# Performance work log

Measured on AMD Instinct MI355X. Metric: run time of the kernel, lower is better.

The kernel has to match this reference:

```python
import jax, jax.numpy as jnp
import numpy as np

N = 25000      # nodes
E = 400000     # edges
IN = 1024      # in_channels
FC = 128       # feature_channels
ADD = 20       # additional_channels
MID = (FC + ADD) // 4   # 37, fc1 output (heads=4)
OUT = 3
EPS = 1e-5
NEG_SLOPE = 0.01


def setup_inputs() -> dict:
    key = jax.random.key(0)
    ks = jax.random.split(key, 16)
    d = {}
    d["features"] = jax.random.normal(ks[0], (N, IN), dtype=jnp.float32)
    d["edges"] = jax.random.randint(ks[1], (2, E), 0, N, dtype=jnp.int64)
    d["edges2"] = jax.random.randint(ks[2], (2, 1000), 0, N, dtype=jnp.int64)
    d["edge_features"] = jax.random.normal(ks[3], (E, 1), dtype=jnp.float32)
    d["additional_feature"] = jax.random.normal(ks[4], (N, ADD), dtype=jnp.float32)
    # SAGEConv params: lin_l (neighbor path, with bias), lin_r (root path, no bias)
    s = 1.0 / np.sqrt(IN)
    d["Wl"] = jax.random.uniform(ks[5], (FC, IN), jnp.float32, -s, s)
    d["bl"] = jax.random.uniform(ks[6], (FC,), jnp.float32, -s, s)
    d["Wr"] = jax.random.uniform(ks[7], (FC, IN), jnp.float32, -s, s)
    s1 = 1.0 / np.sqrt(FC + ADD)
    d["W1"] = jax.random.uniform(ks[8], (MID, FC + ADD), jnp.float32, -s1, s1)
    d["b1"] = jax.random.uniform(ks[9], (MID,), jnp.float32, -s1, s1)
    s2 = 1.0 / np.sqrt(MID)
    d["W2"] = jax.random.uniform(ks[10], (OUT, MID), jnp.float32, -s2, s2)
    d["b2"] = jax.random.uniform(ks[11], (OUT,), jnp.float32, -s2, s2)
    # BatchNorm1d (eval mode -> running stats)
    d["gamma"] = jnp.ones((MID,), jnp.float32)
    d["beta"] = jnp.zeros((MID,), jnp.float32)
    d["run_mean"] = jax.random.normal(ks[12], (MID,), dtype=jnp.float32) * 0.1
    d["run_var"] = jnp.abs(jax.random.normal(ks[13], (MID,), dtype=jnp.float32)) * 0.1 + 1.0
    return d


def reference(features, edges, edges2, edge_features, additional_feature,
              Wl, bl, Wr, W1, b1, W2, b2, gamma, beta, run_mean, run_var):
    src, dst = edges[0], edges[1]  # PyG: messages flow source -> target
    # scatter-mean of neighbor features onto targets
    agg = jax.ops.segment_sum(features[src], dst, num_segments=N)        # [N, IN]
    deg = jax.ops.segment_sum(jnp.ones((E,), features.dtype), dst, num_segments=N)
    agg = agg / jnp.maximum(deg, 1.0)[:, None]
    # SAGEConv: lin_l(mean_neigh) + lin_r(x)
    x = agg @ Wl.T + bl + features @ Wr.T                                 # [N, FC]
    x = jnp.where(x >= 0, x, NEG_SLOPE * x)                               # leaky_relu
    # dropout is identity in eval mode
    x = jnp.concatenate([x, additional_feature], axis=1) @ W1.T + b1      # [N, MID]
    x = jnp.maximum(x, 0.0)                                               # relu
    x = gamma * (x - run_mean) * jax.lax.rsqrt(run_var + EPS) + beta      # BN eval
    return x @ W2.T + b2                                                  # [N, OUT]
```

## Files before the change

kernel.cpp:

```cpp
#include <hip/hip_runtime.h>

#define N_NODES 25000
#define N_EDGES 400000
#define IN_CH 1024
#define FC 128
#define ADD_CH 20
#define XCH 148
#define MID 37
#define OUT_CH 3
#define MAXDEG 64
#define CSTRIDE 16

typedef short bf16x8 __attribute__((ext_vector_type(8)));
typedef float f32x4 __attribute__((ext_vector_type(4)));

__device__ __forceinline__ float bflo(unsigned int v) {
    return __builtin_bit_cast(float, v << 16);
}
__device__ __forceinline__ float bfhi(unsigned int v) {
    return __builtin_bit_cast(float, v & 0xffff0000u);
}
__device__ __forceinline__ unsigned int cvtpk(float a, float b) {
    unsigned int r;
    asm("v_cvt_pk_bf16_f32 %0, %1, %2" : "=v"(r) : "v"(a), "v"(b));
    return r;
}

__device__ __forceinline__ void gload16(const void* g, void* l) {
    __builtin_amdgcn_global_load_lds(
        (const __attribute__((address_space(1))) unsigned int*)g,
        (__attribute__((address_space(3))) unsigned int*)l,
        16, 0, 0);
}

#define WSWZ_B 16
#define ZERO_B 49

__global__ __launch_bounds__(512) void prep(const float* __restrict__ Wl,
                                            const float* __restrict__ Wr,
                                            ushort* __restrict__ Wpk,
                                            int* __restrict__ cursor) {
    int b = blockIdx.x, t = threadIdx.x;
    if (b < WSWZ_B) {
        int w = t >> 6, lane = t & 63, l15 = lane & 15, q8 = (lane >> 4) * 8;
        int ch = b * 16 + l15;
        const float* src = (ch < FC) ? (Wl + (size_t)ch * IN_CH)
                                     : (Wr + (size_t)(ch - FC) * IN_CH);
        #pragma unroll
        for (int j = 0; j < 4; ++j) {
            int kt = w * 4 + j;
            float4 lo = *(const float4*)(src + kt * 32 + q8);
            float4 hi = *(const float4*)(src + kt * 32 + q8 + 4);
            uint4 pk;
            pk.x = cvtpk(lo.x, lo.y); pk.y = cvtpk(lo.z, lo.w);
            pk.z = cvtpk(hi.x, hi.y); pk.w = cvtpk(hi.z, hi.w);
            ((uint4*)Wpk)[((size_t)kt * 16 + b) * 64 + lane] = pk;
        }
    } else {
        int i = (b - WSWZ_B) * 512 + t;
        if (i < N_NODES) {
            uint4 z = {0, 0, 0, 0};
            uint4* dst = (uint4*)(cursor + (size_t)i * CSTRIDE);
            dst[0] = z; dst[1] = z; dst[2] = z; dst[3] = z;
        }
    }
}

#define GEMM_B 391
#define BUILD_B 196

__global__ __launch_bounds__(512, 4) void gemm_build(const float* __restrict__ A,
                                                     const ushort* __restrict__ Wpk,
                                                     ushort* __restrict__ Py,
                                                     ushort* __restrict__ Pz,
                                                     const int* __restrict__ edges,
                                                     int* __restrict__ cursor,
                                                     int* __restrict__ col) {
    __shared__ uint4 LDS[3][1536];
    int b = blockIdx.x, t = threadIdx.x;
    if (b >= GEMM_B) {
        int base = (b - GEMM_B) * 2048 + t;
        int src[4], dst[4], pos[4];
        #pragma unroll
        for (int k = 0; k < 4; ++k) {
            int e = base + k * 512;
            bool v = (e < N_EDGES);
            dst[k] = v ? edges[N_EDGES + e] : 0;
            src[k] = v ? edges[e] : 0;
        }
        #pragma unroll
        for (int k = 0; k < 4; ++k) {
            int e = base + k * 512;
            if (e < N_EDGES)
                pos[k] = atomicAdd(&cursor[(size_t)dst[k] * CSTRIDE], 1);
        }
        #pragma unroll
        for (int k = 0; k < 4; ++k) {
            int e = base + k * 512;
            if (e < N_EDGES && pos[k] < MAXDEG)
                col[dst[k] * MAXDEG + pos[k]] = src[k];
        }
        return;
    }
    int m0 = b * 64;

    int ga = t >> 7, hq = (t >> 6) & 1, la = t & 63;
    int nodeA = m0 + ga * 16 + (la & 15);
    if (nodeA >= N_NODES) nodeA = N_NODES - 1;
    const float* Asrc = A + (size_t)nodeA * IN_CH + (la >> 4) * 8 + hq * 4;
    const uint4* Wg = (const uint4*)Wpk;
    int tb = t & ~63;

    int w = t >> 6, lane = t & 63;
    int wm = w >> 2, wn = w & 3;
    int l15 = lane & 15, q = lane >> 4;

    f32x4 acc[4][2] = {};

    gload16(Wg + t,        &LDS[0][tb]);
    gload16(Wg + 512 + t,  &LDS[0][512 + tb]);
    gload16(Asrc,          &LDS[0][1024 + tb]);
    gload16(Wg + 1024 + t,       &LDS[1][tb]);
    gload16(Wg + 1024 + 512 + t, &LDS[1][512 + tb]);
    gload16(Asrc + 32,           &LDS[1][1024 + tb]);

    #define COMPUTE(bc)                                                           \
    {                                                                             \
        bf16x8 wf[4];                                                             \
        _Pragma("unroll")                                                         \
        for (int i = 0; i < 4; ++i)                                               \
            wf[i] = *(const bf16x8*)&LDS[bc][(wn * 4 + i) * 64 + lane];           \
        bf16x8 af[2];                                                             \
        _Pragma("unroll")                                                         \
        for (int g2 = 0; g2 < 2; ++g2) {                                          \
            f32x4 lo = *(const f32x4*)&LDS[bc][1024 + ((wm * 2 + g2) * 2 + 0) * 64 + lane]; \
            f32x4 hi = *(const f32x4*)&LDS[bc][1024 + ((wm * 2 + g2) * 2 + 1) * 64 + lane]; \
            uint4 pk;                                                             \
            pk.x = cvtpk(lo[0], lo[1]); pk.y = cvtpk(lo[2], lo[3]);               \
            pk.z = cvtpk(hi[0], hi[1]); pk.w = cvtpk(hi[2], hi[3]);               \
            af[g2] = __builtin_bit_cast(bf16x8, pk);                              \
        }                                                                         \
        _Pragma("unroll")                                                         \
        for (int i = 0; i < 4; ++i)                                               \
            _Pragma("unroll")                                                     \
            for (int g2 = 0; g2 < 2; ++g2)                                        \
                acc[i][g2] = __builtin_amdgcn_mfma_f32_16x16x32_bf16(wf[i], af[g2], acc[i][g2], 0, 0, 0); \
    }

    int bc = 0, bs = 2;
    for (int c = 0; c < 30; ++c) {
        const uint4* ws = Wg + (size_t)(c + 2) * 1024;
        gload16(ws + t,       &LDS[bs][tb]);
        gload16(ws + 512 + t, &LDS[bs][512 + tb]);
        gload16(Asrc + (size_t)(c + 2) * 32, &LDS[bs][1024 + tb]);
        asm volatile("s_waitcnt vmcnt(6)" ::: "memory");
        __builtin_amdgcn_sched_barrier(0);
        __builtin_amdgcn_s_barrier();
        __builtin_amdgcn_sched_barrier(0);
        COMPUTE(bc);
        __builtin_amdgcn_s_barrier();
        __builtin_amdgcn_sched_barrier(0);
        bc = (bc == 2) ? 0 : bc + 1;
        bs = (bs == 2) ? 0 : bs + 1;
    }
    asm volatile("s_waitcnt vmcnt(3)" ::: "memory");
    __builtin_amdgcn_sched_barrier(0);
    __builtin_amdgcn_s_barrier();
    __builtin_amdgcn_sched_barrier(0);
    COMPUTE(bc);
    bc = (bc == 2) ? 0 : bc + 1;
    asm volatile("s_waitcnt vmcnt(0)" ::: "memory");
    __builtin_amdgcn_sched_barrier(0);
    __builtin_amdgcn_s_barrier();
    __builtin_amdgcn_sched_barrier(0);
    COMPUTE(bc);
    #undef COMPUTE

    #pragma unroll
    for (int g2 = 0; g2 < 2; ++g2) {
        int node = m0 + wm * 32 + g2 * 16 + l15;
        if (node < N_NODES) {
            ushort* base = (wn < 2) ? (Py + (size_t)node * FC + (wn & 1) * 64 + q * 4)
                                    : (Pz + (size_t)node * FC + (wn & 1) * 64 + q * 4);
            #pragma unroll
            for (int i = 0; i < 4; ++i) {
                f32x4 v = acc[i][g2];
                uint2 pk;
                pk.x = cvtpk(v[0], v[1]);
                pk.y = cvtpk(v[2], v[3]);
                *(uint2*)(base + i * 16) = pk;
            }
        }
    }
}

__global__ __launch_bounds__(512) void fused_tail(const ushort* __restrict__ Py,
                                                  const ushort* __restrict__ Pz,
                                                  const int* __restrict__ deg,
                                                  const int* __restrict__ col,
                                                  const float* __restrict__ addf,
                                                  const float* __restrict__ bl,
                                                  const float* __restrict__ W1,
                                                  const float* __restrict__ b1,
                                                  const float* __restrict__ W2,
                                                  const float* __restrict__ b2,
                                                  const float* __restrict__ gamma,
                                                  const float* __restrict__ beta,
                                                  const float* __restrict__ rmean,
                                                  const float* __restrict__ rvar,
                                                  float* __restrict__ out) {
    __shared__ float W1s[XCH][MID + 3];
    __shared__ float xbuf[8][XCH + 4];
    __shared__ float hbuf[8][MID + 3];
    int t = threadIdx.x;
    for (int idx = t; idx < MID * XCH; idx += 512) {
        int j = idx / XCH, k = idx - j * XCH;
        W1s[k][j] = W1[idx];
    }
    __syncthreads();
    int w = t >> 6, lane = t & 63;
    int n = blockIdx.x * 8 + w;
    bool valid = (n < N_NODES);
    int d = valid ? deg[(size_t)n * CSTRIDE] : 0;
    if (d > MAXDEG) d = MAXDEG;
    int g = lane >> 4, c16 = lane & 15;
    float s[8] = {0.f, 0.f, 0.f, 0.f, 0.f, 0.f, 0.f, 0.f};
    if (d > 0) {
        int cidx = col[n * MAXDEG + (lane < d ? lane : 0)];
        for (int i = 0; i < d; i += 16) {
            int e[4];
            uint4 v[4];
            #pragma unroll
            for (int j = 0; j < 4; ++j) {
                int ee = i + g + j * 4;
                e[j] = __shfl(cidx, (ee < d) ? ee : 0);
            }
            #pragma unroll
            for (int j = 0; j < 4; ++j)
                v[j] = *(const uint4*)&Py[(size_t)e[j] * FC + c16 * 8];
            #pragma unroll
            for (int j = 0; j < 4; ++j) {
                if (i + g + j * 4 < d) {
                    s[0] += bflo(v[j].x); s[1] += bfhi(v[j].x);
                    s[2] += bflo(v[j].y); s[3] += bfhi(v[j].y);
                    s[4] += bflo(v[j].z); s[5] += bfhi(v[j].z);
                    s[6] += bflo(v[j].w); s[7] += bfhi(v[j].w);
                }
            }
        }
        #pragma unroll
        for (int r = 0; r < 8; ++r) {
            s[r] += __shfl_xor(s[r], 16);
            s[r] += __shfl_xor(s[r], 32);
        }
    }
    if (valid) {
        if (lane < 16) {
            #pragma unroll
            for (int r = 0; r < 8; ++r) xbuf[w][lane * 8 + r] = s[r];
        }
        float invd = 1.0f / (float)(d > 1 ? d : 1);
        unsigned int vr = *(const unsigned int*)&Pz[(size_t)n * FC + lane * 2];
        float x0 = xbuf[w][2 * lane] * invd + bl[2 * lane] + bflo(vr);
        float x1 = xbuf[w][2 * lane + 1] * invd + bl[2 * lane + 1] + bfhi(vr);
        x0 = (x0 >= 0.f) ? x0 : 0.01f * x0;
        x1 = (x1 >= 0.f) ? x1 : 0.01f * x1;
        xbuf[w][2 * lane] = x0;
        xbuf[w][2 * lane + 1] = x1;
        if (lane < ADD_CH) xbuf[w][FC + lane] = addf[(size_t)n * ADD_CH + lane];
        if (lane < MID) {
            float h = b1[lane];
            #pragma unroll 4
            for (int k = 0; k < XCH; ++k) h += W1s[k][lane] * xbuf[w][k];
            h = fmaxf(h, 0.0f);
            h = gamma[lane] * (h - rmean[lane]) * rsqrtf(rvar[lane] + 1e-5f) + beta[lane];
            hbuf[w][lane] = h;
        }
        if (lane < OUT_CH) {
            float o = b2[lane];
            #pragma unroll
            for (int j = 0; j < MID; ++j) o += W2[lane * MID + j] * hbuf[w][j];
            out[(size_t)n * OUT_CH + lane] = o;
        }
    }
}


extern "C" void kernel_launch(void* const* d_in, const int* in_sizes, int n_in,
                              void* d_out, int out_size, void* d_ws, size_t ws_size,
                              hipStream_t stream) {
    const float* features = (const float*)d_in[0];
    const int*   edges    = (const int*)d_in[1];
    const float* addf     = (const float*)d_in[4];
    const float* Wl       = (const float*)d_in[5];
    const float* bl       = (const float*)d_in[6];
    const float* Wr       = (const float*)d_in[7];
    const float* W1       = (const float*)d_in[8];
    const float* b1       = (const float*)d_in[9];
    const float* W2       = (const float*)d_in[10];
    const float* b2       = (const float*)d_in[11];
    const float* gamma    = (const float*)d_in[12];
    const float* beta     = (const float*)d_in[13];
    const float* rmean    = (const float*)d_in[14];
    const float* rvar     = (const float*)d_in[15];
    float* out = (float*)d_out;

    char* ws = (char*)d_ws;
    size_t off = 0;
    ushort* Py = (ushort*)(ws + off);     off += (size_t)N_NODES * FC * 2;
    ushort* Pz = (ushort*)(ws + off);     off += (size_t)N_NODES * FC * 2;
    ushort* Wpk = (ushort*)(ws + off);    off += (size_t)32 * 16 * 64 * 16;
    int* cursor = (int*)(ws + off);       off += (size_t)N_NODES * CSTRIDE * 4;
    int* col = (int*)(ws + off);          off += (size_t)N_NODES * MAXDEG * 4;

    prep<<<WSWZ_B + ZERO_B, 512, 0, stream>>>(Wl, Wr, Wpk, cursor);

    gemm_build<<<GEMM_B + BUILD_B, 512, 0, stream>>>(features, Wpk, Py, Pz,
                                                     edges, cursor, col);

    fused_tail<<<(N_NODES + 7) / 8, 512, 0, stream>>>(Py, Pz, cursor, col, addf, bl,
                                                      W1, b1, W2, b2, gamma, beta,
                                                      rmean, rvar, out);
}
```

Measured before the change: 255.0 us.

## Load weight fragments directly into registers and repartition warps over output columns

Weight tiles are no longer staged through LDS. Each wave now loads its own weight fragments straight into VGPRs with global_load_dwordx4, triple-buffered in registers, and only the fp32 A tile stays in LDS. The wave-to-output mapping changes so each wave covers all 64 rows and 32 output columns, which removes the LDS reads and writes for weights and shrinks LDS to a third. In exchange it uses more registers per thread for the in-flight weight buffers, and every wave re-reads the shared A tile from LDS four times, which may affect occupancy and LDS bandwidth.

```diff
diff --git a/kernel.cpp b/kernel.cpp
--- a/kernel.cpp
+++ b/kernel.cpp
@@ -13,6 +13,7 @@
 
 typedef short bf16x8 __attribute__((ext_vector_type(8)));
 typedef float f32x4 __attribute__((ext_vector_type(4)));
+typedef unsigned int u32x4 __attribute__((ext_vector_type(4)));
 
 __device__ __forceinline__ float bflo(unsigned int v) {
     return __builtin_bit_cast(float, v << 16);
@@ -76,7 +77,7 @@
                                                      const int* __restrict__ edges,
                                                      int* __restrict__ cursor,
                                                      int* __restrict__ col) {
-    __shared__ uint4 LDS[3][1536];
+    __shared__ uint4 LDS[3][512];
     int b = blockIdx.x, t = threadIdx.x;
     if (b >= GEMM_B) {
         int base = (b - GEMM_B) * 2048 + t;
@@ -103,92 +104,93 @@
         return;
     }
     int m0 = b * 64;
-
-    int ga = t >> 7, hq = (t >> 6) & 1, la = t & 63;
-    int nodeA = m0 + ga * 16 + (la & 15);
+    int w = t >> 6, lane = t & 63;
+    int l15 = lane & 15, q = lane >> 4;
+    int tb = t & ~63;
+
+    int ga = t >> 7, hq = (t >> 6) & 1;
+    int nodeA = m0 + ga * 16 + l15;
     if (nodeA >= N_NODES) nodeA = N_NODES - 1;
-    const float* Asrc = A + (size_t)nodeA * IN_CH + (la >> 4) * 8 + hq * 4;
-    const uint4* Wg = (const uint4*)Wpk;
-    int tb = t & ~63;
-
-    int w = t >> 6, lane = t & 63;
-    int wm = w >> 2, wn = w & 3;
-    int l15 = lane & 15, q = lane >> 4;
-
-    f32x4 acc[4][2] = {};
-
-    gload16(Wg + t,        &LDS[0][tb]);
-    gload16(Wg + 512 + t,  &LDS[0][512 + tb]);
-    gload16(Asrc,          &LDS[0][1024 + tb]);
-    gload16(Wg + 1024 + t,       &LDS[1][tb]);
-    gload16(Wg + 1024 + 512 + t, &LDS[1][512 + tb]);
-    gload16(Asrc + 32,           &LDS[1][1024 + tb]);
-
-    #define COMPUTE(bc)                                                           \
+    const float* Asrc = A + (size_t)nodeA * IN_CH + q * 8 + hq * 4;
+
+    unsigned voff0 = (unsigned)(w * 128 + lane) * 16u;
+
+    f32x4 acc[2][4] = {};
+    u32x4 wA0, wA1, wB0, wB1, wC0, wC1;
+
+    #define ISSUE_W(R0, R1, vo)                                                   \
+        asm volatile("global_load_dwordx4 %0, %2, %3\n\t"                         \
+                     "global_load_dwordx4 %1, %2, %3 offset:1024"                 \
+                     : "=&v"(R0), "=&v"(R1) : "v"(vo), "s"(Wpk) : "memory");
+
+    gload16(Asrc, &LDS[0][tb]);
+    ISSUE_W(wA0, wA1, voff0)
+    gload16(Asrc + 32, &LDS[1][tb]);
+    { unsigned vo = voff0 + 16384u; ISSUE_W(wB0, wB1, vo) }
+
+    #define COMPUTE(W0r, W1r, cb)                                                 \
     {                                                                             \
-        bf16x8 wf[4];                                                             \
+        bf16x8 wf0 = __builtin_bit_cast(bf16x8, W0r);                             \
+        bf16x8 wf1 = __builtin_bit_cast(bf16x8, W1r);                             \
         _Pragma("unroll")                                                         \
-        for (int i = 0; i < 4; ++i)                                               \
-            wf[i] = *(const bf16x8*)&LDS[bc][(wn * 4 + i) * 64 + lane];           \
-        bf16x8 af[2];                                                             \
-        _Pragma("unroll")                                                         \
-        for (int g2 = 0; g2 < 2; ++g2) {                                          \
-            f32x4 lo = *(const f32x4*)&LDS[bc][1024 + ((wm * 2 + g2) * 2 + 0) * 64 + lane]; \
-            f32x4 hi = *(const f32x4*)&LDS[bc][1024 + ((wm * 2 + g2) * 2 + 1) * 64 + lane]; \
-            uint4 pk;                                                             \
-            pk.x = cvtpk(lo[0], lo[1]); pk.y = cvtpk(lo[2], lo[3]);               \
-            pk.z = cvtpk(hi[0], hi[1]); pk.w = cvtpk(hi[2], hi[3]);               \
-            af[g2] = __builtin_bit_cast(bf16x8, pk);                              \
+        for (int g = 0; g < 4; ++g) {                                             \
+            f32x4 lo = *(const f32x4*)&LDS[cb][g * 128 + lane];                   \
+            f32x4 hi = *(const f32x4*)&LDS[cb][g * 128 + 64 + lane];              \
+            uint4 pk_;                                                            \
+            pk_.x = cvtpk(lo[0], lo[1]); pk_.y = cvtpk(lo[2], lo[3]);             \
+            pk_.z = cvtpk(hi[0], hi[1]); pk_.w = cvtpk(hi[2], hi[3]);             \
+            bf16x8 af = __builtin_bit_cast(bf16x8, pk_);                          \
+            acc[0][g] = __builtin_amdgcn_mfma_f32_16x16x32_bf16(wf0, af, acc[0][g], 0, 0, 0); \
+            acc[1][g] = __builtin_amdgcn_mfma_f32_16x16x32_bf16(wf1, af, acc[1][g], 0, 0, 0); \
         }                                                                         \
-        _Pragma("unroll")                                                         \
-        for (int i = 0; i < 4; ++i)                                               \
-            _Pragma("unroll")                                                     \
-            for (int g2 = 0; g2 < 2; ++g2)                                        \
-                acc[i][g2] = __builtin_amdgcn_mfma_f32_16x16x32_bf16(wf[i], af[g2], acc[i][g2], 0, 0, 0); \
-    }
-
-    int bc = 0, bs = 2;
-    for (int c = 0; c < 30; ++c) {
-        const uint4* ws = Wg + (size_t)(c + 2) * 1024;
-        gload16(ws + t,       &LDS[bs][tb]);
-        gload16(ws + 512 + t, &LDS[bs][512 + tb]);
-        gload16(Asrc + (size_t)(c + 2) * 32, &LDS[bs][1024 + tb]);
-        asm volatile("s_waitcnt vmcnt(6)" ::: "memory");
-        __builtin_amdgcn_sched_barrier(0);
-        __builtin_amdgcn_s_barrier();
-        __builtin_amdgcn_sched_barrier(0);
-        COMPUTE(bc);
-        __builtin_amdgcn_s_barrier();
-        __builtin_amdgcn_sched_barrier(0);
-        bc = (bc == 2) ? 0 : bc + 1;
-        bs = (bs == 2) ? 0 : bs + 1;
+    }
+
+    #define STEP(c, WS0, WS1, WC0, WC1, SBUF, CBUF)                               \
+    {                                                                             \
+        gload16(Asrc + (size_t)((c) + 2) * 32, &LDS[SBUF][tb]);                   \
+        unsigned vo = voff0 + (unsigned)((c) + 2) * 16384u;                       \
+        ISSUE_W(WS0, WS1, vo)                                                     \
+        asm volatile("s_waitcnt vmcnt(6)" ::: "memory");                          \
+        __builtin_amdgcn_sched_barrier(0);                                        \
+        __builtin_amdgcn_s_barrier();                                             \
+        __builtin_amdgcn_sched_barrier(0);                                        \
+        COMPUTE(WC0, WC1, CBUF);                                                  \
+        __builtin_amdgcn_s_barrier();                                             \
+        __builtin_amdgcn_sched_barrier(0);                                        \
+    }
+
+    for (int cc = 0; cc < 30; cc += 3) {
+        STEP(cc,     wC0, wC1, wA0, wA1, 2, 0)
+        STEP(cc + 1, wA0, wA1, wB0, wB1, 0, 1)
+        STEP(cc + 2, wB0, wB1, wC0, wC1, 1, 2)
     }
     asm volatile("s_waitcnt vmcnt(3)" ::: "memory");
     __builtin_amdgcn_sched_barrier(0);
     __builtin_amdgcn_s_barrier();
     __builtin_amdgcn_sched_barrier(0);
-    COMPUTE(bc);
-    bc = (bc == 2) ? 0 : bc + 1;
+    COMPUTE(wA0, wA1, 0);
     asm volatile("s_waitcnt vmcnt(0)" ::: "memory");
     __builtin_amdgcn_sched_barrier(0);
     __builtin_amdgcn_s_barrier();
     __builtin_amdgcn_sched_barrier(0);
-    COMPUTE(bc);
+    COMPUTE(wB0, wB1, 1);
+    #undef STEP
     #undef COMPUTE
+    #undef ISSUE_W
 
     #pragma unroll
-    for (int g2 = 0; g2 < 2; ++g2) {
-        int node = m0 + wm * 32 + g2 * 16 + l15;
+    for (int g = 0; g < 4; ++g) {
+        int node = m0 + g * 16 + l15;
         if (node < N_NODES) {
-            ushort* base = (wn < 2) ? (Py + (size_t)node * FC + (wn & 1) * 64 + q * 4)
-                                    : (Pz + (size_t)node * FC + (wn & 1) * 64 + q * 4);
-            #pragma unroll
-            for (int i = 0; i < 4; ++i) {
-                f32x4 v = acc[i][g2];
+            ushort* base = (w < 4) ? (Py + (size_t)node * FC + w * 32 + q * 4)
+                                   : (Pz + (size_t)node * FC + (w - 4) * 32 + q * 4);
+            #pragma unroll
+            for (int cf = 0; cf < 2; ++cf) {
+                f32x4 v = acc[cf][g];
                 uint2 pk;
                 pk.x = cvtpk(v[0], v[1]);
                 pk.y = cvtpk(v[2], v[3]);
-                *(uint2*)(base + i * 16) = pk;
+                *(uint2*)(base + cf * 16) = pk;
             }
         }
     }
```

After: 270.4 us. +6.1%, slower.
